# Performance work log

Hardware: AMD Instinct MI355X
Metric: run time of the kernel (lower is better)

Reference implementation:

```python
import jax, jax.numpy as jnp
import numpy as np

H = 16  # num_attention_heads
D = 64  # attention_head_size


def setup_inputs() -> dict:
    key = jax.random.key(0)
    ks = jax.random.split(key, 10)
    B, S, Hid = 8, 512, 1024
    scale = 0.02
    hidden_states = jax.random.normal(ks[0], (B, S, Hid), jnp.float32)
    attention_mask = jnp.zeros((B, 1, 1, S), jnp.float32)
    graph_emb = jax.random.randint(ks[1], (B, S, S), 0, 3, jnp.int32)
    Wq = jax.random.normal(ks[2], (Hid, Hid), jnp.float32) * scale
    bq = jnp.zeros((Hid,), jnp.float32)
    Wk = jax.random.normal(ks[3], (Hid, Hid), jnp.float32) * scale
    bk = jnp.zeros((Hid,), jnp.float32)
    Wv = jax.random.normal(ks[4], (Hid, Hid), jnp.float32) * scale
    bv = jnp.zeros((Hid,), jnp.float32)
    dp_k = jax.random.normal(ks[5], (3, D), jnp.float32) * scale
    dp_v = jax.random.normal(ks[6], (3, D), jnp.float32) * scale
    return {"hidden_states": hidden_states, "attention_mask": attention_mask,
            "graph_emb": graph_emb, "Wq": Wq, "bq": bq, "Wk": Wk, "bk": bk,
            "Wv": Wv, "bv": bv, "dp_k": dp_k, "dp_v": dp_v}


def reference(hidden_states, attention_mask, graph_emb, Wq, bq, Wk, bk, Wv, bv, dp_k, dp_v):
    B, S, Hid = hidden_states.shape

    def proj(W, b):  # nn.Linear: x @ W.T + b, then split heads -> [B,H,S,D]
        y = hidden_states @ W.T + b
        return y.reshape(B, S, H, D).transpose(0, 2, 1, 3)

    q = proj(Wq, bq)
    k = proj(Wk, bk)
    v = proj(Wv, bv)

    # padding_idx=0 -> row 0 of relation tables is zero
    dp_k = dp_k.at[0].set(0.0)
    dp_v = dp_v.at[0].set(0.0)
    dp_keys = dp_k[graph_emb]    # [B,S,S,D]
    dp_values = dp_v[graph_emb]  # [B,S,S,D]

    scores = jnp.einsum('bhqd,bhkd->bhqk', q, k) / jnp.sqrt(jnp.float32(D))
    scores = scores + jnp.einsum('bhqd,bqkd->bhqk', q, dp_keys)  # relative_matmul_dp
    scores = scores + attention_mask
    probs = jax.nn.softmax(scores, axis=-1)

    ctx = jnp.einsum('bhqk,bhkd->bhqd', probs, v)
    ctx = ctx + jnp.einsum('bhqk,bqkd->bhqd', probs, dp_values)  # relative_matmul_dpv
    return ctx.transpose(0, 2, 1, 3).reshape(B, S, H * D)
```

## Files before the change

kernel.cpp:

```cpp
#include <hip/hip_runtime.h>
#include <hip/hip_bf16.h>
#include <cstddef>

#define B_  8
#define S_  512
#define HID 1024
#define H_  16
#define D_  64

typedef float f32x4 __attribute__((ext_vector_type(4)));
typedef _Float16 f16x8 __attribute__((ext_vector_type(8)));
typedef short s16x8 __attribute__((ext_vector_type(8)));
typedef unsigned short u16t;

__device__ __forceinline__ u16t f2h(float v) {
    return __builtin_bit_cast(u16t, (_Float16)v);
}
__device__ __forceinline__ float h2f(u16t u) {
    return (float)__builtin_bit_cast(_Float16, u);
}

__device__ __forceinline__ void gll16(const u16t* g, u16t* l) {
    __builtin_amdgcn_global_load_lds(
        (const __attribute__((address_space(1))) unsigned int*)(const void*)g,
        (__attribute__((address_space(3))) unsigned int*)(void*)l, 16, 0, 0);
}

__global__ __launch_bounds__(256) void conv_all_kernel(
    const float* __restrict__ X,
    const float* __restrict__ Wq, const float* __restrict__ Wk,
    const float* __restrict__ Wv,
    u16t* __restrict__ Xh, u16t* __restrict__ Wh)
{
    const int nX4 = (B_ * S_ * HID) / 4;
    const int nW4 = (HID * HID) / 4;
    int i = blockIdx.x * 256 + threadIdx.x;
    const float* src;
    u16t* dst;
    int off;
    if (i < nX4)                { src = X;  dst = Xh;                         off = i; }
    else if (i < nX4 + nW4)     { src = Wq; dst = Wh;                         off = i - nX4; }
    else if (i < nX4 + 2 * nW4) { src = Wk; dst = Wh + (size_t)HID * HID;     off = i - nX4 - nW4; }
    else                        { src = Wv; dst = Wh + (size_t)2 * HID * HID; off = i - nX4 - 2 * nW4; }
    float4 x = ((const float4*)src)[off];
    ushort4 h;
    h.x = f2h(x.x);
    h.y = f2h(x.y);
    h.z = f2h(x.z);
    h.w = f2h(x.w);
    ((ushort4*)dst)[off] = h;
}

__global__ __launch_bounds__(256) void qkv_mfma_kernel(
    const u16t* __restrict__ Xhi, const u16t* __restrict__ Whi,
    const float* __restrict__ bq, const float* __restrict__ bk,
    const float* __restrict__ bv,
    u16t* __restrict__ Qh, u16t* __restrict__ Kh, u16t* __restrict__ Vth)
{
    const int which = blockIdx.z;
    const u16t* __restrict__ WhiB = Whi + (size_t)which * (HID * HID);
    const float* __restrict__ bias = (which == 0) ? bq : (which == 1) ? bk : bv;

    __shared__ __align__(16) u16t SM[2 * 8192];
    u16t* const Ah = SM;
    u16t* const Bh = SM + 8192;

    const int tid  = threadIdx.x;
    const int lane = tid & 63;
    const int wv_  = tid >> 6;
    const int wr   = wv_ >> 1;
    const int wc   = wv_ & 1;
    const int m0   = blockIdx.y * 128;
    const int n0   = blockIdx.x * 128;

    f32x4 acc[4][4];
    #pragma unroll
    for (int mi = 0; mi < 4; ++mi)
        #pragma unroll
        for (int ni = 0; ni < 4; ++ni)
            #pragma unroll
            for (int e = 0; e < 4; ++e) acc[mi][ni][e] = 0.0f;

    const int rowB0 = wv_ * 32 + (lane >> 3);
    const int ch    = (lane & 7) ^ (rowB0 & 7);
    const size_t aof = (size_t)(m0 + rowB0) * HID + ch * 8;
    const size_t bof = (size_t)(n0 + rowB0) * HID + ch * 8;

    const int colL = lane & 15;
    const int kg   = lane >> 4;
    const int sx   = colL & 7;
    const int arow = (wr * 64 + colL) * 64;
    const int brow = (wc * 64 + colL) * 64;

    for (int k0 = 0; k0 < HID; k0 += 64) {
        __syncthreads();
        #pragma unroll
        for (int s = 0; s < 4; ++s) {
            gll16(&Xhi [aof + k0 + (size_t)(s * 8) * HID], Ah + (wv_ * 32 + s * 8) * 64);
            gll16(&WhiB[bof + k0 + (size_t)(s * 8) * HID], Bh + (wv_ * 32 + s * 8) * 64);
        }
        __syncthreads();

        #pragma unroll
        for (int ks = 0; ks < 2; ++ks) {
            const int so = ((ks * 4 + kg) ^ sx) * 8;
            f16x8 a_[4], b_[4];
            #pragma unroll
            for (int mi = 0; mi < 4; ++mi)
                a_[mi] = *(const f16x8*)&Ah[arow + mi * 1024 + so];
            #pragma unroll
            for (int ni = 0; ni < 4; ++ni)
                b_[ni] = *(const f16x8*)&Bh[brow + ni * 1024 + so];
            #pragma unroll
            for (int mi = 0; mi < 4; ++mi)
                #pragma unroll
                for (int ni = 0; ni < 4; ++ni)
                    acc[mi][ni] = __builtin_amdgcn_mfma_f32_16x16x32_f16(
                        a_[mi], b_[ni], acc[mi][ni], 0, 0, 0);
        }
    }

    if (which == 2) {
        #pragma unroll
        for (int mi = 0; mi < 4; ++mi) {
            #pragma unroll
            for (int ni = 0; ni < 4; ++ni) {
                const int n    = n0 + wc * 64 + ni * 16 + colL;
                const int mrow = m0 + wr * 64 + mi * 16 + kg * 4;
                const float bn = bias[n];
                const int bb = mrow >> 9;
                const int ss = mrow & (S_ - 1);
                const int hh = n >> 6;
                const int dd = n & (D_ - 1);
                ushort4 vh;
                vh.x = f2h(acc[mi][ni][0] + bn);
                vh.y = f2h(acc[mi][ni][1] + bn);
                vh.z = f2h(acc[mi][ni][2] + bn);
                vh.w = f2h(acc[mi][ni][3] + bn);
                *(ushort4*)&Vth[(((size_t)bb * H_ + hh) * D_ + dd) * S_ + ss] = vh;
            }
        }
    } else {
        u16t* __restrict__ Oh = (which == 0) ? Qh : Kh;
        float* LF = (float*)SM;
        float bn4[4];
        #pragma unroll
        for (int ni = 0; ni < 4; ++ni) bn4[ni] = bias[n0 + wc * 64 + ni * 16 + colL];

        const int er  = tid >> 3;
        const int ecc = (tid & 7) * 16;
        const int ehh = (n0 + ecc) >> 6;
        const int edd = ecc & 63;
        const int mrowE = m0 + (er >> 4) * 64 + (er & 15);

        #pragma unroll
        for (int mi = 0; mi < 4; ++mi) {
            __syncthreads();
            #pragma unroll
            for (int ni = 0; ni < 4; ++ni)
                #pragma unroll
                for (int j = 0; j < 4; ++j)
                    LF[(wr * 16 + kg * 4 + j) * 130 + wc * 64 + ni * 16 + colL] =
                        acc[mi][ni][j] + bn4[ni];
            __syncthreads();

            const int mrow = mrowE + mi * 16;
            const int bb = mrow >> 9;
            const int ss = mrow & (S_ - 1);
            __align__(16) u16t hv[16];
            #pragma unroll
            for (int u = 0; u < 16; u += 4) {
                float4 v = *(const float4*)&LF[er * 130 + ecc + u];
                hv[u + 0] = f2h(v.x);
                hv[u + 1] = f2h(v.y);
                hv[u + 2] = f2h(v.z);
                hv[u + 3] = f2h(v.w);
            }
            const size_t off = (((size_t)bb * H_ + ehh) * S_ + ss) * D_ + edd;
            *(s16x8*)&Oh[off]     = *(const s16x8*)&hv[0];
            *(s16x8*)&Oh[off + 8] = *(const s16x8*)&hv[8];
        }
    }
}

__global__ __launch_bounds__(512) void attn_mfma_kernel(
    const u16t* __restrict__ Qhg, const u16t* __restrict__ Khg,
    const u16t* __restrict__ Vhg,
    const int*  __restrict__ ge,  const float* __restrict__ mask,
    const float* __restrict__ dpk, const float* __restrict__ dpv,
    float* __restrict__ out)
{
    __shared__ __align__(16) u16t Q_s[128 * 64];
    __shared__ __align__(16) u16t K_s[64 * 64];
    __shared__ __align__(16) u16t V_s[64 * 64];
    __shared__ __align__(16) u16t P_s[8 * 2304];

    const int tid  = threadIdx.x;
    const int lane = tid & 63;
    const int wq   = tid >> 6;
    const int c    = lane & 15;
    const int g    = lane >> 4;
    const int sx   = c & 7;
    const int bid  = blockIdx.x;
    const int bh   = bid >> 2;
    const int q0   = (bid & 3) * 128;
    const int b    = bh >> 4;
    const int h    = bh & (H_ - 1);

    u16t* Pw = &P_s[wq * 2304];

    {
        const u16t* qbase = Qhg + ((size_t)bh * S_ + q0) * D_;
        #pragma unroll
        for (int t = 0; t < 2; ++t) {
            const int chk = tid + t * 512;
            const int r = chk >> 3, s = chk & 7;
            *(s16x8*)&Q_s[r * 64 + ((s ^ (r & 7)) << 3)] =
                *(const s16x8*)&qbase[chk * 8];
        }
    }

    const int r_   = tid >> 3;
    const int s_   = tid & 7;
    const int ldso = r_ * 64 + ((s_ ^ (r_ & 7)) << 3);
    const u16t* kgp = &Khg[((size_t)bh * S_ + r_) * D_ + s_ * 8];
    const u16t* vgp = &Vhg[((size_t)bh * D_ + r_) * S_ + s_ * 8];

    {
        s16x8 kr = *(const s16x8*)kgp;
        s16x8 vr = *(const s16x8*)vgp;
        *(s16x8*)&K_s[ldso] = kr;
        *(s16x8*)&V_s[ldso] = vr;
    }
    __syncthreads();

    float tq1, tq2;
    {
        const int qrow = wq * 16 + c;
        float a1 = 0.f, a2 = 0.f;
        #pragma unroll
        for (int t = 0; t < 2; ++t) {
            const int slot = 2 * g + t;
            const f16x8 qv8 = *(const f16x8*)&Q_s[qrow * 64 + ((slot ^ sx) << 3)];
            const int dbase = slot * 8;
            #pragma unroll
            for (int i = 0; i < 8; ++i) {
                const float qv = (float)qv8[i];
                a1 = fmaf(qv, dpk[D_ + dbase + i], a1);
                a2 = fmaf(qv, dpk[2 * D_ + dbase + i], a2);
            }
        }
        a1 += __shfl_xor(a1, 16); a1 += __shfl_xor(a1, 32);
        a2 += __shfl_xor(a2, 16); a2 += __shfl_xor(a2, 32);
        tq1 = a1; tq2 = a2;
    }

    const size_t geoff = ((size_t)b * S_ + q0 + wq * 16 + c) * S_;
    const float* mrow = &mask[(size_t)b * S_];

    float mrun = -INFINITY, lrun = 0.f, w1 = 0.f, w2 = 0.f;
    f32x4 ctx4[4];
    #pragma unroll
    for (int mi = 0; mi < 4; ++mi)
        #pragma unroll
        for (int e = 0; e < 4; ++e) ctx4[mi][e] = 0.f;

    for (int kt = 0; kt < S_ / 64; ++kt) {
        const int k0 = kt * 64;

        s16x8 krB, vrB;
        if (kt < S_ / 64 - 1) {
            krB = *(const s16x8*)(kgp + (size_t)(k0 + 64) * D_);
            vrB = *(const s16x8*)(vgp + (k0 + 64));
        }

        f32x4 s4[4];
        #pragma unroll
        for (int mi = 0; mi < 4; ++mi)
            #pragma unroll
            for (int e = 0; e < 4; ++e) s4[mi][e] = 0.f;

        #pragma unroll
        for (int ks = 0; ks < 2; ++ks) {
            const int so = ((g + 4 * ks) ^ sx) << 3;
            const f16x8 qh_ = *(const f16x8*)&Q_s[(wq * 16 + c) * 64 + so];
            #pragma unroll
            for (int mi = 0; mi < 4; ++mi) {
                const f16x8 kh_ = *(const f16x8*)&K_s[(mi * 16 + c) * 64 + so];
                s4[mi] = __builtin_amdgcn_mfma_f32_16x16x32_f16(kh_, qh_, s4[mi], 0, 0, 0);
            }
        }

        float sv[4][4];
        int   gcode[4][4];
        float tmax = -INFINITY;
        #pragma unroll
        for (int mi = 0; mi < 4; ++mi) {
            const int4   gc = *(const int4*)&ge[geoff + k0 + mi * 16 + g * 4];
            const float4 mk = *(const float4*)&mrow[k0 + mi * 16 + g * 4];
            const int   gg[4] = {gc.x, gc.y, gc.z, gc.w};
            const float mm[4] = {mk.x, mk.y, mk.z, mk.w};
            #pragma unroll
            for (int j = 0; j < 4; ++j) {
                const float t = (gg[j] == 1) ? tq1 : (gg[j] == 2) ? tq2 : 0.f;
                const float x = fmaf(s4[mi][j], 0.125f, t + mm[j]);
                sv[mi][j] = x;
                gcode[mi][j] = gg[j];
                tmax = fmaxf(tmax, x);
            }
        }
        tmax = fmaxf(tmax, __shfl_xor(tmax, 16));
        tmax = fmaxf(tmax, __shfl_xor(tmax, 32));

        const float mn    = fmaxf(mrun, tmax);
        const float alpha = __expf(mrun - mn);
        mrun = mn;

        float rs = 0.f, rb1 = 0.f, rb2 = 0.f;
        #pragma unroll
        for (int mi = 0; mi < 4; ++mi)
            #pragma unroll
            for (int j = 0; j < 4; ++j) {
                const float e = __expf(sv[mi][j] - mn);
                sv[mi][j] = e;
                rs += e;
                rb1 += (gcode[mi][j] == 1) ? e : 0.f;
                rb2 += (gcode[mi][j] == 2) ? e : 0.f;
            }
        rs  += __shfl_xor(rs, 16);  rs  += __shfl_xor(rs, 32);
        rb1 += __shfl_xor(rb1, 16); rb1 += __shfl_xor(rb1, 32);
        rb2 += __shfl_xor(rb2, 16); rb2 += __shfl_xor(rb2, 32);

        lrun = lrun * alpha + rs;
        w1   = w1   * alpha + rb1;
        w2   = w2   * alpha + rb2;
        #pragma unroll
        for (int mi = 0; mi < 4; ++mi) ctx4[mi] *= alpha;

        #pragma unroll
        for (int mi = 0; mi < 4; ++mi) {
            ushort4 ph;
            ph.x = f2h(sv[mi][0]);
            ph.y = f2h(sv[mi][1]);
            ph.z = f2h(sv[mi][2]);
            ph.w = f2h(sv[mi][3]);
            const int slotp = (2 * mi + (g >> 1)) ^ sx;
            *(ushort4*)&Pw[c * 64 + slotp * 8 + (g & 1) * 4] = ph;
        }

        #pragma unroll
        for (int ks = 0; ks < 2; ++ks) {
            const int so = ((g + 4 * ks) ^ sx) << 3;
            const f16x8 ph_ = *(const f16x8*)&Pw[c * 64 + so];
            #pragma unroll
            for (int mi = 0; mi < 4; ++mi) {
                const f16x8 vh_ = *(const f16x8*)&V_s[(mi * 16 + c) * 64 + so];
                ctx4[mi] = __builtin_amdgcn_mfma_f32_16x16x32_f16(vh_, ph_, ctx4[mi], 0, 0, 0);
            }
        }
        __syncthreads();

        if (kt < S_ / 64 - 1) {
            *(s16x8*)&K_s[ldso] = krB;
            *(s16x8*)&V_s[ldso] = vrB;
            __syncthreads();
        }
    }

    const float inv = 1.0f / lrun;
    float* tb = (float*)&P_s[wq * 2304];
    #pragma unroll
    for (int mi = 0; mi < 4; ++mi) {
        const float4 dk1 = *(const float4*)&dpv[D_ + mi * 16 + g * 4];
        const float4 dk2 = *(const float4*)&dpv[2 * D_ + mi * 16 + g * 4];
        const float a1[4] = {dk1.x, dk1.y, dk1.z, dk1.w};
        const float a2[4] = {dk2.x, dk2.y, dk2.z, dk2.w};
        #pragma unroll
        for (int j = 0; j < 4; ++j) {
            const float val = (ctx4[mi][j] + w1 * a1[j] + w2 * a2[j]) * inv;
            tb[(mi * 16 + g * 4 + j) * 17 + c] = val;
        }
    }
    __syncthreads();
    #pragma unroll
    for (int qq = 0; qq < 16; ++qq)
        out[((size_t)b * S_ + q0 + wq * 16 + qq) * (H_ * D_) + h * D_ + lane] =
            tb[lane * 17 + qq];
}

extern "C" void kernel_launch(void* const* d_in, const int* in_sizes, int n_in,
                              void* d_out, int out_size, void* d_ws, size_t ws_size,
                              hipStream_t stream)
{
    const float* hs   = (const float*)d_in[0];
    const float* mask = (const float*)d_in[1];
    const int*   ge   = (const int*)d_in[2];
    const float* Wq   = (const float*)d_in[3];
    const float* bq   = (const float*)d_in[4];
    const float* Wk   = (const float*)d_in[5];
    const float* bk   = (const float*)d_in[6];
    const float* Wv   = (const float*)d_in[7];
    const float* bv   = (const float*)d_in[8];
    const float* dpk  = (const float*)d_in[9];
    const float* dpv  = (const float*)d_in[10];
    float* out = (float*)d_out;

    const size_t per = (size_t)B_ * H_ * S_ * D_;
    const size_t nX  = (size_t)B_ * S_ * HID;
    const size_t nW  = (size_t)HID * HID;

    u16t* base = (u16t*)d_ws;
    u16t* Qh  = base;
    u16t* Kh  = Qh  + per;
    u16t* Vth = Kh  + per;
    u16t* Xhi = Vth + per;
    u16t* Whi = Xhi + nX;

    const int nConv = (int)((nX + 3 * nW) / 4);
    conv_all_kernel<<<nConv / 256, 256, 0, stream>>>(hs, Wq, Wk, Wv, Xhi, Whi);

    dim3 gridG(HID / 128, (B_ * S_) / 128, 3);
    qkv_mfma_kernel<<<gridG, dim3(256), 0, stream>>>(
        Xhi, Whi, bq, bk, bv, Qh, Kh, Vth);

    dim3 gridB(B_ * H_ * (S_ / 128));
    attn_mfma_kernel<<<gridB, dim3(512), 0, stream>>>(
        Qh, Kh, Vth, ge, mask, dpk, dpv, out);
}
```

Before: 89.67 us.

## Double-buffer QKV GEMM loads and add lazy softmax rescaling with MFMA priority

The QKV projection GEMM now double-buffers its LDS tiles. The next K-slice is prefetched with global_load_lds while the current one is being multiplied, which removes one barrier per iteration. The attention kernel now issues the graph-code and mask loads before the QK MFMAs. It skips the online-softmax rescale of the accumulators unless the running max grows by more than 8. It also raises wave priority around the MFMA blocks. The lazy rescale risks larger fp16 probability values, and the extra LDS buffer may reduce occupancy.

```diff
diff --git a/kernel.cpp b/kernel.cpp
--- a/kernel.cpp
+++ b/kernel.cpp
@@ -61,9 +61,7 @@
     const u16t* __restrict__ WhiB = Whi + (size_t)which * (HID * HID);
     const float* __restrict__ bias = (which == 0) ? bq : (which == 1) ? bk : bv;
 
-    __shared__ __align__(16) u16t SM[2 * 8192];
-    u16t* const Ah = SM;
-    u16t* const Bh = SM + 8192;
+    __shared__ __align__(16) u16t SM[2 * 16384];
 
     const int tid  = threadIdx.x;
     const int lane = tid & 63;
@@ -85,6 +83,7 @@
     const int ch    = (lane & 7) ^ (rowB0 & 7);
     const size_t aof = (size_t)(m0 + rowB0) * HID + ch * 8;
     const size_t bof = (size_t)(n0 + rowB0) * HID + ch * 8;
+    const int ldsA = (wv_ * 32) * 64;
 
     const int colL = lane & 15;
     const int kg   = lane >> 4;
@@ -92,14 +91,24 @@
     const int arow = (wr * 64 + colL) * 64;
     const int brow = (wc * 64 + colL) * 64;
 
+    #pragma unroll
+    for (int s = 0; s < 4; ++s) {
+        gll16(&Xhi [aof + (size_t)(s * 8) * HID], SM + ldsA + s * 512);
+        gll16(&WhiB[bof + (size_t)(s * 8) * HID], SM + 8192 + ldsA + s * 512);
+    }
+    __syncthreads();
+
     for (int k0 = 0; k0 < HID; k0 += 64) {
-        __syncthreads();
-        #pragma unroll
-        for (int s = 0; s < 4; ++s) {
-            gll16(&Xhi [aof + k0 + (size_t)(s * 8) * HID], Ah + (wv_ * 32 + s * 8) * 64);
-            gll16(&WhiB[bof + k0 + (size_t)(s * 8) * HID], Bh + (wv_ * 32 + s * 8) * 64);
-        }
-        __syncthreads();
+        const int cur = (k0 >> 6) & 1;
+        u16t* const bufc = SM + cur * 16384;
+        if (k0 + 64 < HID) {
+            u16t* const bufn = SM + (cur ^ 1) * 16384;
+            #pragma unroll
+            for (int s = 0; s < 4; ++s) {
+                gll16(&Xhi [aof + k0 + 64 + (size_t)(s * 8) * HID], bufn + ldsA + s * 512);
+                gll16(&WhiB[bof + k0 + 64 + (size_t)(s * 8) * HID], bufn + 8192 + ldsA + s * 512);
+            }
+        }
 
         #pragma unroll
         for (int ks = 0; ks < 2; ++ks) {
@@ -107,10 +116,10 @@
             f16x8 a_[4], b_[4];
             #pragma unroll
             for (int mi = 0; mi < 4; ++mi)
-                a_[mi] = *(const f16x8*)&Ah[arow + mi * 1024 + so];
+                a_[mi] = *(const f16x8*)&bufc[arow + mi * 1024 + so];
             #pragma unroll
             for (int ni = 0; ni < 4; ++ni)
-                b_[ni] = *(const f16x8*)&Bh[brow + ni * 1024 + so];
+                b_[ni] = *(const f16x8*)&bufc[8192 + brow + ni * 1024 + so];
             #pragma unroll
             for (int mi = 0; mi < 4; ++mi)
                 #pragma unroll
@@ -118,6 +127,7 @@
                     acc[mi][ni] = __builtin_amdgcn_mfma_f32_16x16x32_f16(
                         a_[mi], b_[ni], acc[mi][ni], 0, 0, 0);
         }
+        __syncthreads();
     }
 
     if (which == 2) {
@@ -273,6 +283,13 @@
             krB = *(const s16x8*)(kgp + (size_t)(k0 + 64) * D_);
             vrB = *(const s16x8*)(vgp + (k0 + 64));
         }
+        int4   gc4[4];
+        float4 mk4[4];
+        #pragma unroll
+        for (int mi = 0; mi < 4; ++mi) {
+            gc4[mi] = *(const int4*)&ge[geoff + k0 + mi * 16 + g * 4];
+            mk4[mi] = *(const float4*)&mrow[k0 + mi * 16 + g * 4];
+        }
 
         f32x4 s4[4];
         #pragma unroll
@@ -280,6 +297,7 @@
             #pragma unroll
             for (int e = 0; e < 4; ++e) s4[mi][e] = 0.f;
 
+        __builtin_amdgcn_s_setprio(1);
         #pragma unroll
         for (int ks = 0; ks < 2; ++ks) {
             const int so = ((g + 4 * ks) ^ sx) << 3;
@@ -290,16 +308,15 @@
                 s4[mi] = __builtin_amdgcn_mfma_f32_16x16x32_f16(kh_, qh_, s4[mi], 0, 0, 0);
             }
         }
+        __builtin_amdgcn_s_setprio(0);
 
         float sv[4][4];
         int   gcode[4][4];
         float tmax = -INFINITY;
         #pragma unroll
         for (int mi = 0; mi < 4; ++mi) {
-            const int4   gc = *(const int4*)&ge[geoff + k0 + mi * 16 + g * 4];
-            const float4 mk = *(const float4*)&mrow[k0 + mi * 16 + g * 4];
-            const int   gg[4] = {gc.x, gc.y, gc.z, gc.w};
-            const float mm[4] = {mk.x, mk.y, mk.z, mk.w};
+            const int   gg[4] = {gc4[mi].x, gc4[mi].y, gc4[mi].z, gc4[mi].w};
+            const float mm[4] = {mk4[mi].x, mk4[mi].y, mk4[mi].z, mk4[mi].w};
             #pragma unroll
             for (int j = 0; j < 4; ++j) {
                 const float t = (gg[j] == 1) ? tq1 : (gg[j] == 2) ? tq2 : 0.f;
@@ -312,16 +329,21 @@
         tmax = fmaxf(tmax, __shfl_xor(tmax, 16));
         tmax = fmaxf(tmax, __shfl_xor(tmax, 32));
 
-        const float mn    = fmaxf(mrun, tmax);
-        const float alpha = __expf(mrun - mn);
-        mrun = mn;
+        if (!__all(tmax - mrun <= 8.0f)) {
+            const float mn    = fmaxf(mrun, tmax);
+            const float alpha = __expf(mrun - mn);
+            mrun = mn;
+            lrun *= alpha; w1 *= alpha; w2 *= alpha;
+            #pragma unroll
+            for (int mi = 0; mi < 4; ++mi) ctx4[mi] *= alpha;
+        }
 
         float rs = 0.f, rb1 = 0.f, rb2 = 0.f;
         #pragma unroll
         for (int mi = 0; mi < 4; ++mi)
             #pragma unroll
             for (int j = 0; j < 4; ++j) {
-                const float e = __expf(sv[mi][j] - mn);
+                const float e = __expf(sv[mi][j] - mrun);
                 sv[mi][j] = e;
                 rs += e;
                 rb1 += (gcode[mi][j] == 1) ? e : 0.f;
@@ -331,11 +353,9 @@
         rb1 += __shfl_xor(rb1, 16); rb1 += __shfl_xor(rb1, 32);
         rb2 += __shfl_xor(rb2, 16); rb2 += __shfl_xor(rb2, 32);
 
-        lrun = lrun * alpha + rs;
-        w1   = w1   * alpha + rb1;
-        w2   = w2   * alpha + rb2;
-        #pragma unroll
-        for (int mi = 0; mi < 4; ++mi) ctx4[mi] *= alpha;
+        lrun += rs;
+        w1   += rb1;
+        w2   += rb2;
 
         #pragma unroll
         for (int mi = 0; mi < 4; ++mi) {
@@ -348,6 +368,7 @@
             *(ushort4*)&Pw[c * 64 + slotp * 8 + (g & 1) * 4] = ph;
         }
 
+        __builtin_amdgcn_s_setprio(1);
         #pragma unroll
         for (int ks = 0; ks < 2; ++ks) {
             const int so = ((g + 4 * ks) ^ sx) << 3;
@@ -358,6 +379,7 @@
                 ctx4[mi] = __builtin_amdgcn_mfma_f32_16x16x32_f16(vh_, ph_, ctx4[mi], 0, 0, 0);
             }
         }
+        __builtin_amdgcn_s_setprio(0);
         __syncthreads();
 
         if (kt < S_ / 64 - 1) {
```

Measured after the change: 79.65 us. 1.13x faster.
